# Kernel tuning notes

Measured on AMD Instinct MI355X. Metric: run time of the kernel, lower is better.

## Reference

```python
import jax, jax.numpy as jnp
import numpy as np

B, N, D = 4, 1024, 64
H, DH = 8, 64
INNER = H * DH  # 512 == dim*heads
NUM_F, GH, GW = 4, 16, 16  # N = GH*GW*NUM_F
EPS_LN = 1e-5


def setup_inputs() -> dict:
    key = jax.random.key(0)
    ks = jax.random.split(key, 5)
    return {
        "x": jax.random.normal(ks[0], (B, N, D), dtype=jnp.float32),
        "W_qkv": jax.random.normal(ks[1], (D, 3 * INNER), dtype=jnp.float32) * 0.05,
        "b_qkv": jax.random.normal(ks[2], (3 * INNER,), dtype=jnp.float32) * 0.02,
        "ln_g": jnp.ones((INNER,), dtype=jnp.float32),
        "ln_b": jnp.zeros((INNER,), dtype=jnp.float32),
        "W_out": jax.random.normal(ks[3], (INNER, D), dtype=jnp.float32) * 0.05,
        "b_out": jnp.zeros((D,), dtype=jnp.float32),
    }


def _safe_sqrt(d2):
    # sqrt with zero (not inf) gradient at 0 (diagonal of cdist)
    pos = d2 > 1e-12
    return jnp.where(pos, jnp.sqrt(jnp.where(pos, d2, 1.0)), 0.0)


def _spe_weights(x):
    # torch.cdist(x, x, p=2) then Gaussian kernel, thresholded at mean
    sq = jnp.sum(x * x, axis=-1)  # (B,N)
    d2 = sq[:, :, None] + sq[:, None, :] - 2.0 * jnp.einsum('bnd,bmd->bnm', x, x)
    d2 = jnp.maximum(d2, 0.0)
    dist = _safe_sqrt(d2)
    sigma = jnp.mean(dist)
    w = jnp.exp(-d2 / (2.0 * sigma * sigma))
    return jnp.where(w < jnp.mean(w), 0.0, w)  # (B,N,N)


def _spa_weights():
    # constant spatial-grid Gaussian weights, identical across batch
    gx, gy, gz = jnp.meshgrid(jnp.arange(GH), jnp.arange(GW), jnp.arange(NUM_F), indexing='ij')
    grid = jnp.stack([gx, gy, gz], axis=-1).reshape(N, 3).astype(jnp.float32)
    diff = grid[:, None, :] - grid[None, :, :]
    d2 = jnp.sum(diff * diff, axis=-1)
    dist = jnp.sqrt(d2)
    sigma = jnp.mean(dist)
    w = jnp.exp(-d2 / (2.0 * sigma * sigma))
    return jnp.where(w < jnp.mean(w), 0.0, w)  # (N,N)


def reference(x, W_qkv, b_qkv, ln_g, ln_b, W_out, b_out):
    spe = _spe_weights(x)            # (B,N,N), broadcast over heads
    spa = _spa_weights()             # (N,N), broadcast over batch & heads

    qkv = x @ W_qkv + b_qkv          # (B,N,3*INNER)
    q, k, v = jnp.split(qkv, 3, axis=-1)
    to_heads = lambda t: t.reshape(B, N, H, DH).transpose(0, 2, 1, 3)  # (B,H,N,DH)
    q, k, v = to_heads(q), to_heads(k), to_heads(v)

    scale = DH ** (-0.5)
    qe = jax.nn.elu(q) + 1.0
    ke = jax.nn.elu(k) + 1.0
    dots = jnp.einsum('bhid,bhjd->bhij', qe, ke) * scale  # (B,H,N,N)

    masked = dots * spe[:, None, :, :] * spa[None, None, :, :]
    attn = jax.nn.softmax(masked, axis=-1)
    out = jnp.einsum('bhij,bhjd->bhid', attn, v)          # (B,H,N,DH)
    out = out.transpose(0, 2, 1, 3).reshape(B, N, INNER)

    # to_out: LayerNorm -> GELU (exact) -> Linear
    mu = jnp.mean(out, axis=-1, keepdims=True)
    var = jnp.var(out, axis=-1, keepdims=True)
    y = ln_g * (out - mu) / jnp.sqrt(var + EPS_LN) + ln_b
    y = jax.nn.gelu(y, approximate=False)
    return y @ W_out + b_out  # (B,N,D)
```

## Files before the change

kernel.cpp:

```cpp
#include <hip/hip_runtime.h>
#include <math.h>
#include <stdlib.h>

#define B 4
#define N 1024
#define D 64
#define H 8
#define DH 64
#define INNER 512
#define C3 1536
#define BHN 32768
#define BHND 2097152

typedef __attribute__((ext_vector_type(8))) short bf16x8;
typedef __attribute__((ext_vector_type(4))) float f32x4;

__device__ inline short f2bf(float f) {
    unsigned u = __builtin_bit_cast(unsigned, f);
    unsigned r = (u + 0x7FFFu + ((u >> 16) & 1u)) >> 16;
    return (short)r;
}
__device__ inline float bf2f(short s) {
    return __builtin_bit_cast(float, ((unsigned)(unsigned short)s) << 16);
}

__global__ __launch_bounds__(256) void k_prep(const float* __restrict__ x, const float* __restrict__ Wqkv,
                                              short* __restrict__ xh, short* __restrict__ xl,
                                              float* __restrict__ sq,
                                              short* __restrict__ Wh, short* __restrict__ Wl,
                                              float* __restrict__ spa, float inv2s2, float mu,
                                              float* __restrict__ scal) {
    __shared__ float lds[64 * 65];
    int t = threadIdx.x;
    int bb = blockIdx.x;
    if (bb < 1024) {
        if (bb == 0 && t < 16) scal[t] = 0.f;
        int i = bb * 4 + (t >> 6), d = t & 63;
        float v = x[i * 64 + d];
        short hs = f2bf(v);
        xh[i * 64 + d] = hs;
        xl[i * 64 + d] = f2bf(v - bf2f(hs));
        float s = v * v;
#pragma unroll
        for (int m = 32; m; m >>= 1) s += __shfl_xor(s, m, 64);
        if (d == 0) sq[i] = s;
    } else if (bb < 1048) {
        int c0 = (bb - 1024) * 64;
#pragma unroll
        for (int it = 0; it < 16; it++) {
            int d = it * 4 + (t >> 6), cl = t & 63;
            lds[cl * 65 + d] = Wqkv[d * C3 + c0 + cl];
        }
        __syncthreads();
#pragma unroll
        for (int it = 0; it < 16; it++) {
            int cl = it * 4 + (t >> 6), d = t & 63;
            float v = lds[cl * 65 + d];
            short hs = f2bf(v);
            Wh[(c0 + cl) * 64 + d] = hs;
            Wl[(c0 + cl) * 64 + d] = f2bf(v - bf2f(hs));
        }
    } else {
        int flat4 = (bb - 1048) * 256 + t;
        int i = flat4 >> 8;
        int j0 = (flat4 & 255) * 4;
        int ix = i >> 6, iy = (i >> 2) & 15, iz = i & 3;
        float4 o;
        float* op = (float*)&o;
#pragma unroll
        for (int jj = 0; jj < 4; jj++) {
            int j = j0 + jj;
            int jx = j >> 6, jy = (j >> 2) & 15, jz = j & 3;
            float d2 = (float)((ix - jx) * (ix - jx) + (iy - jy) * (iy - jy) + (iz - jz) * (iz - jz));
            float w = __expf(-d2 * inv2s2);
            op[jj] = (w < mu) ? 0.f : w;
        }
        ((float4*)spa)[flat4] = o;
    }
}

__global__ __launch_bounds__(256) void k_gemm(
    const short* __restrict__ xh, const short* __restrict__ xl,
    const short* __restrict__ Wh, const short* __restrict__ Wl,
    const float* __restrict__ bqkv, const float* __restrict__ sq,
    short* __restrict__ qeh, short* __restrict__ qel,
    short* __restrict__ keh, short* __restrict__ kel,
    short* __restrict__ vT, float* __restrict__ w, float* __restrict__ d_sig) {
    __shared__ short vt_lds[128 * 66];
    __shared__ float red[4];
    int t = threadIdx.x;
    int wv = t >> 6, lane = t & 63, l4 = lane & 15, g = lane >> 4;
    const bf16x8* xh8 = (const bf16x8*)xh;
    const bf16x8* xl8 = (const bf16x8*)xl;

    if (blockIdx.x < 768) {
        int i0 = (blockIdx.x & 63) * 64;
        int c0 = (blockIdx.x >> 6) * 128;
        int irow = i0 + wv * 16;
        const bf16x8* Wh8 = (const bf16x8*)Wh;
        const bf16x8* Wl8 = (const bf16x8*)Wl;
        int abase = (irow + l4) * 8 + g;
        bf16x8 ah[2], al[2];
        ah[0] = xh8[abase];
        ah[1] = xh8[abase + 4];
        al[0] = xl8[abase];
        al[1] = xl8[abase + 4];
        f32x4 acc[8];
#pragma unroll
        for (int ct = 0; ct < 8; ct++) {
            int c = c0 + 16 * ct + l4;
            int bbase = c * 8 + g;
            bf16x8 bh0 = Wh8[bbase], bh1 = Wh8[bbase + 4];
            bf16x8 bl0 = Wl8[bbase], bl1 = Wl8[bbase + 4];
            f32x4 a = f32x4{0.f, 0.f, 0.f, 0.f};
            a = __builtin_amdgcn_mfma_f32_16x16x32_bf16(ah[0], bh0, a, 0, 0, 0);
            a = __builtin_amdgcn_mfma_f32_16x16x32_bf16(ah[1], bh1, a, 0, 0, 0);
            a = __builtin_amdgcn_mfma_f32_16x16x32_bf16(al[0], bh0, a, 0, 0, 0);
            a = __builtin_amdgcn_mfma_f32_16x16x32_bf16(al[1], bh1, a, 0, 0, 0);
            a = __builtin_amdgcn_mfma_f32_16x16x32_bf16(ah[0], bl0, a, 0, 0, 0);
            a = __builtin_amdgcn_mfma_f32_16x16x32_bf16(ah[1], bl1, a, 0, 0, 0);
            acc[ct] = a;
        }
        int seg = c0 >> 9;
#pragma unroll
        for (int ct = 0; ct < 8; ct++) {
            int c = c0 + 16 * ct + l4;
            float bias = bqkv[c];
            int cc = c & 511, hh = cc >> 6, dh = cc & 63;
#pragma unroll
            for (int r = 0; r < 4; r++) {
                int i_e = irow + 4 * g + r;
                int b = i_e >> 10, i = i_e & 1023;
                float val = acc[ct][r] + bias;
                if (seg < 2) {
                    float a_ = val > 0.f ? val + 1.f : __expf(val);
                    short hs = f2bf(a_);
                    short ls = f2bf(a_ - bf2f(hs));
                    int off = ((b * H + hh) * N + i) * 64 + dh;
                    if (seg == 0) { qeh[off] = hs; qel[off] = ls; }
                    else          { keh[off] = hs; kel[off] = ls; }
                } else {
                    vt_lds[(16 * ct + l4) * 66 + (wv * 16 + 4 * g + r)] = f2bf(val);
                }
            }
        }
        if (seg == 2) {
            __syncthreads();
            int b = i0 >> 10, ib = i0 & 1023;
#pragma unroll
            for (int it = 0; it < 4; it++) {
                int idx = t + 256 * it;
                int cl = idx >> 3, i8 = idx & 7;
                short tmp[8];
#pragma unroll
                for (int r8 = 0; r8 < 8; r8++) tmp[r8] = vt_lds[cl * 66 + i8 * 8 + r8];
                int cc = (c0 + cl) & 511, hh = cc >> 6, dh = cc & 63;
                ((bf16x8*)vT)[((b * H + hh) * 64 + dh) * (N / 8) + (ib >> 3) + i8] = *(bf16x8*)tmp;
            }
        }
    } else {
        int q = blockIdx.x - 768;
        int i0 = (q & 15) * 64, j0 = ((q >> 4) & 7) * 128, b = q >> 7;
        int irow = i0 + wv * 16;
        int abase = (b * N + irow + l4) * 8 + g;
        bf16x8 ah[2], al[2];
        ah[0] = xh8[abase];
        ah[1] = xh8[abase + 4];
        al[0] = xl8[abase];
        al[1] = xl8[abase + 4];
        f32x4 acc[8];
#pragma unroll
        for (int ct = 0; ct < 8; ct++) {
            int j = j0 + 16 * ct + l4;
            int bbase = (b * N + j) * 8 + g;
            bf16x8 bh0 = xh8[bbase], bh1 = xh8[bbase + 4];
            bf16x8 bl0 = xl8[bbase], bl1 = xl8[bbase + 4];
            f32x4 a = f32x4{0.f, 0.f, 0.f, 0.f};
            a = __builtin_amdgcn_mfma_f32_16x16x32_bf16(ah[0], bh0, a, 0, 0, 0);
            a = __builtin_amdgcn_mfma_f32_16x16x32_bf16(ah[1], bh1, a, 0, 0, 0);
            a = __builtin_amdgcn_mfma_f32_16x16x32_bf16(al[0], bh0, a, 0, 0, 0);
            a = __builtin_amdgcn_mfma_f32_16x16x32_bf16(al[1], bh1, a, 0, 0, 0);
            a = __builtin_amdgcn_mfma_f32_16x16x32_bf16(ah[0], bl0, a, 0, 0, 0);
            a = __builtin_amdgcn_mfma_f32_16x16x32_bf16(ah[1], bl1, a, 0, 0, 0);
            acc[ct] = a;
        }
        float sqi[4];
#pragma unroll
        for (int r = 0; r < 4; r++) sqi[r] = sq[b * N + irow + 4 * g + r];
        float part = 0.f;
#pragma unroll
        for (int ct = 0; ct < 8; ct++) {
            int j = j0 + 16 * ct + l4;
            float sqj = sq[b * N + j];
#pragma unroll
            for (int r = 0; r < 4; r++) {
                float d2 = sqi[r] + sqj - 2.f * acc[ct][r];
                d2 = fmaxf(d2, 0.f);
                w[((size_t)b * N + irow + 4 * g + r) * N + j] = d2;
                part += (d2 > 1e-12f) ? sqrtf(d2) : 0.f;
            }
        }
#pragma unroll
        for (int m = 32; m; m >>= 1) part += __shfl_xor(part, m, 64);
        if (lane == 0) red[wv] = part;
        __syncthreads();
        if (t == 0) atomicAdd(d_sig, red[0] + red[1] + red[2] + red[3]);
    }
}

__global__ __launch_bounds__(256) void k_wsum(const float* __restrict__ w, const float* __restrict__ d_sig,
                                              float* __restrict__ d_wsum) {
    __shared__ float red[4];
    float sigma = d_sig[0] * (1.f / 4194304.f);
    float inv = 1.f / (2.f * sigma * sigma);
    float s = 0.f;
    for (int idx = blockIdx.x * 256 + threadIdx.x; idx < 1048576; idx += 256 * 2048) {
        float4 v = ((const float4*)w)[idx];
        s += __expf(-v.x * inv) + __expf(-v.y * inv) + __expf(-v.z * inv) + __expf(-v.w * inv);
    }
#pragma unroll
    for (int m = 32; m; m >>= 1) s += __shfl_xor(s, m, 64);
    if ((threadIdx.x & 63) == 0) red[threadIdx.x >> 6] = s;
    __syncthreads();
    if (threadIdx.x == 0) atomicAdd(d_wsum, red[0] + red[1] + red[2] + red[3]);
}

__global__ __launch_bounds__(256) void k_attn(
    const short* __restrict__ qeh, const short* __restrict__ qel,
    const short* __restrict__ keh, const short* __restrict__ kel,
    const short* __restrict__ vT,
    const float* __restrict__ w, const float* __restrict__ spa,
    const float* __restrict__ scal, float* __restrict__ Opart, float2* __restrict__ ml2) {
    __shared__ short Kh[64 * 64];
    __shared__ short Kl[64 * 64];
    __shared__ short Vt[64 * 64];
    __shared__ short P[4][16 * 64];
    int t = threadIdx.x;
    int wv = t >> 6, lane = t & 63, l4 = lane & 15, g = lane >> 4;
    int half = blockIdx.x & 1;
    int i0 = (blockIdx.x >> 1) * 64;
    int h = blockIdx.y, b = blockIdx.z, bh = b * H + h;
    float sigma = scal[0] * (1.f / 4194304.f);
    float inv = 1.f / (2.f * sigma * sigma);
    float mu = scal[1] * (1.f / 4194304.f);
    int irow = i0 + wv * 16;

    bf16x8 qh[2], ql[2];
    {
        const bf16x8* qh8 = (const bf16x8*)qeh;
        const bf16x8* ql8 = (const bf16x8*)qel;
        int base = (bh * N + irow + l4) * 8 + g;
#pragma unroll
        for (int mk = 0; mk < 2; mk++) {
            qh[mk] = qh8[base + 4 * mk];
            ql[mk] = ql8[base + 4 * mk];
        }
    }
    f32x4 O[4];
#pragma unroll
    for (int dt = 0; dt < 4; dt++) O[dt] = f32x4{0.f, 0.f, 0.f, 0.f};
    float m_r[4] = {-INFINITY, -INFINITY, -INFINITY, -INFINITY};
    float l_r[4] = {0.f, 0.f, 0.f, 0.f};

    const bf16x8* Kh8 = (const bf16x8*)Kh;
    const bf16x8* Kl8 = (const bf16x8*)Kl;
    const bf16x8* Vt8 = (const bf16x8*)Vt;

    for (int tile = half * 8; tile < half * 8 + 8; ++tile) {
        int j0 = tile * 64;
        __syncthreads();
        {
            const bf16x8* kh8 = (const bf16x8*)keh;
            const bf16x8* kl8 = (const bf16x8*)kel;
            const bf16x8* v8 = (const bf16x8*)vT;
            bf16x8* KhW = (bf16x8*)Kh;
            bf16x8* KlW = (bf16x8*)Kl;
            bf16x8* VtW = (bf16x8*)Vt;
#pragma unroll
            for (int rep = 0; rep < 2; rep++) {
                int c = t + 256 * rep;
                int j = c >> 3, s = c & 7;
                KhW[j * 8 + (s ^ (j & 7))] = kh8[(bh * N + j0 + j) * 8 + s];
                KlW[j * 8 + (s ^ (j & 7))] = kl8[(bh * N + j0 + j) * 8 + s];
                VtW[j * 8 + (s ^ (j & 7))] = v8[(bh * 64 + j) * (N / 8) + (j0 >> 3) + s];
            }
        }
        __syncthreads();
        f32x4 sc[4];
#pragma unroll
        for (int ct = 0; ct < 4; ct++) {
            int j = 16 * ct + l4;
            int sw = j & 7;
            bf16x8 kh0 = Kh8[j * 8 + ((g) ^ sw)];
            bf16x8 kh1 = Kh8[j * 8 + ((4 + g) ^ sw)];
            bf16x8 kl0 = Kl8[j * 8 + ((g) ^ sw)];
            bf16x8 kl1 = Kl8[j * 8 + ((4 + g) ^ sw)];
            f32x4 a = f32x4{0.f, 0.f, 0.f, 0.f};
            a = __builtin_amdgcn_mfma_f32_16x16x32_bf16(qh[0], kh0, a, 0, 0, 0);
            a = __builtin_amdgcn_mfma_f32_16x16x32_bf16(qh[1], kh1, a, 0, 0, 0);
            a = __builtin_amdgcn_mfma_f32_16x16x32_bf16(ql[0], kh0, a, 0, 0, 0);
            a = __builtin_amdgcn_mfma_f32_16x16x32_bf16(ql[1], kh1, a, 0, 0, 0);
            a = __builtin_amdgcn_mfma_f32_16x16x32_bf16(qh[0], kl0, a, 0, 0, 0);
            a = __builtin_amdgcn_mfma_f32_16x16x32_bf16(qh[1], kl1, a, 0, 0, 0);
            sc[ct] = a;
        }
        float p[4][4];
        float fr[4];
#pragma unroll
        for (int r = 0; r < 4; r++) {
            int i = irow + 4 * g + r;
            float mx = -INFINITY;
#pragma unroll
            for (int ct = 0; ct < 4; ct++) {
                int jg = j0 + 16 * ct + l4;
                float d2v = w[((size_t)b * N + i) * N + jg];
                float sp = spa[(size_t)i * N + jg];
                float wv_ = __expf(-d2v * inv);
                float spe = (wv_ < mu) ? 0.f : wv_;
                float val = sc[ct][r] * 0.125f * spe * sp;
                p[ct][r] = val;
                mx = fmaxf(mx, val);
            }
#pragma unroll
            for (int msk = 1; msk < 16; msk <<= 1) mx = fmaxf(mx, __shfl_xor(mx, msk, 64));
            float mo = m_r[r];
            float mn = fmaxf(mo, mx);
            float f = __expf(mo - mn);
            float s = 0.f;
#pragma unroll
            for (int ct = 0; ct < 4; ct++) {
                float e = __expf(p[ct][r] - mn);
                p[ct][r] = e;
                s += e;
            }
#pragma unroll
            for (int msk = 1; msk < 16; msk <<= 1) s += __shfl_xor(s, msk, 64);
            l_r[r] = l_r[r] * f + s;
            m_r[r] = mn;
            fr[r] = f;
        }
#pragma unroll
        for (int dt = 0; dt < 4; dt++) {
            O[dt][0] *= fr[0];
            O[dt][1] *= fr[1];
            O[dt][2] *= fr[2];
            O[dt][3] *= fr[3];
        }
        short* Pw = P[wv];
#pragma unroll
        for (int ct = 0; ct < 4; ct++) {
#pragma unroll
            for (int r = 0; r < 4; r++) {
                int row = 4 * g + r;
                int slot = ((l4 >> 3) + 2 * ct) ^ (row & 7);
                Pw[row * 64 + slot * 8 + (l4 & 7)] = f2bf(p[ct][r]);
            }
        }
        const bf16x8* Pr = (const bf16x8*)P[wv];
#pragma unroll
        for (int ks = 0; ks < 2; ks++) {
            bf16x8 pa = Pr[l4 * 8 + ((g + 4 * ks) ^ (l4 & 7))];
#pragma unroll
            for (int dt = 0; dt < 4; dt++) {
                int d = l4 + 16 * dt;
                bf16x8 bv = Vt8[d * 8 + ((g + 4 * ks) ^ (d & 7))];
                O[dt] = __builtin_amdgcn_mfma_f32_16x16x32_bf16(pa, bv, O[dt], 0, 0, 0);
            }
        }
    }
    float* Op = Opart + (size_t)half * BHND;
#pragma unroll
    for (int dt = 0; dt < 4; dt++) {
#pragma unroll
        for (int r = 0; r < 4; r++) {
            int i = irow + 4 * g + r;
            Op[((size_t)bh * N + i) * 64 + l4 + 16 * dt] = O[dt][r];
        }
    }
    if (l4 == 0) {
#pragma unroll
        for (int r = 0; r < 4; r++)
            ml2[half * BHN + bh * N + irow + 4 * g + r] = float2{m_r[r], l_r[r]};
    }
}

__device__ inline float4 comb4(const float* __restrict__ Opart, const float2* __restrict__ ml2,
                               int bh, int ib, int dq) {
    float2 a0 = ml2[bh * N + ib];
    float2 a1 = ml2[BHN + bh * N + ib];
    float m = fmaxf(a0.x, a1.x);
    float e0 = __expf(a0.x - m), e1 = __expf(a1.x - m);
    float inv = 1.f / (a0.y * e0 + a1.y * e1);
    const float4* Op4 = (const float4*)Opart;
    float4 O0 = Op4[(size_t)(bh * N + ib) * 16 + dq];
    float4 O1 = Op4[(size_t)(BHND / 4) + (size_t)(bh * N + ib) * 16 + dq];
    float4 v;
    v.x = (O0.x * e0 + O1.x * e1) * inv;
    v.y = (O0.y * e0 + O1.y * e1) * inv;
    v.z = (O0.z * e0 + O1.z * e1) * inv;
    v.w = (O0.w * e0 + O1.w * e1) * inv;
    return v;
}

__global__ __launch_bounds__(256) void k_out(const float* __restrict__ Opart, const float2* __restrict__ ml2,
                                             const float* __restrict__ g, const float* __restrict__ be,
                                             const float* __restrict__ Wout, const float* __restrict__ bout,
                                             float* __restrict__ out) {
    __shared__ float y_s[8 * 512];
    int t = threadIdx.x;
    int wv = t >> 6, lane = t & 63;
    int r0 = blockIdx.x * 8;
#pragma unroll
    for (int rr = 0; rr < 2; rr++) {
        int rloc = wv * 2 + rr;
        int ig = r0 + rloc;
        int b = ig >> 10, ib = ig & 1023;
        int c0 = 4 * lane, c1 = c0 + 256;
        float4 v0 = comb4(Opart, ml2, b * H + (c0 >> 6), ib, (c0 & 63) >> 2);
        float4 v1 = comb4(Opart, ml2, b * H + (c1 >> 6), ib, (c1 & 63) >> 2);
        float s1 = v0.x + v0.y + v0.z + v0.w + v1.x + v1.y + v1.z + v1.w;
        float s2 = v0.x * v0.x + v0.y * v0.y + v0.z * v0.z + v0.w * v0.w +
                   v1.x * v1.x + v1.y * v1.y + v1.z * v1.z + v1.w * v1.w;
#pragma unroll
        for (int m = 32; m; m >>= 1) {
            s1 += __shfl_xor(s1, m, 64);
            s2 += __shfl_xor(s2, m, 64);
        }
        float mean = s1 * (1.f / 512.f);
        float var = s2 * (1.f / 512.f) - mean * mean;
        float rstd = rsqrtf(var + 1e-5f);
        float4 o0, o1;
#pragma unroll
        for (int e = 0; e < 4; e++) {
            float yn = g[c0 + e] * (((float*)&v0)[e] - mean) * rstd + be[c0 + e];
            ((float*)&o0)[e] = 0.5f * yn * (1.f + erff(yn * 0.70710678118f));
            float ym = g[c1 + e] * (((float*)&v1)[e] - mean) * rstd + be[c1 + e];
            ((float*)&o1)[e] = 0.5f * ym * (1.f + erff(ym * 0.70710678118f));
        }
        ((float4*)(y_s + rloc * 512))[lane] = o0;
        ((float4*)(y_s + rloc * 512))[lane + 64] = o1;
    }
    __syncthreads();
    int o = t & 63, rg = t >> 6;
    float a0 = 0.f, a1 = 0.f;
#pragma unroll 4
    for (int c = 0; c < 512; c++) {
        float wv_ = Wout[c * 64 + o];
        a0 = fmaf(y_s[(rg * 2) * 512 + c], wv_, a0);
        a1 = fmaf(y_s[(rg * 2 + 1) * 512 + c], wv_, a1);
    }
    float bo = bout[o];
    out[(size_t)(r0 + rg * 2) * 64 + o] = a0 + bo;
    out[(size_t)(r0 + rg * 2 + 1) * 64 + o] = a1 + bo;
}

extern "C" void kernel_launch(void* const* d_in, const int* in_sizes, int n_in,
                              void* d_out, int out_size, void* d_ws, size_t ws_size,
                              hipStream_t stream) {
    const float* x = (const float*)d_in[0];
    const float* Wqkv = (const float*)d_in[1];
    const float* bqkv = (const float*)d_in[2];
    const float* lng = (const float*)d_in[3];
    const float* lnb = (const float*)d_in[4];
    const float* Wout = (const float*)d_in[5];
    const float* bout = (const float*)d_in[6];
    float* out = (float*)d_out;

    float* ws = (float*)d_ws;
    size_t off = 0;
    float* sq = ws + off;    off += (size_t)B * N;
    float* scal = ws + off;  off += 16;
    float* spa = ws + off;   off += (size_t)N * N;
    float* wbuf = ws + off;  off += (size_t)B * N * N;
    float* Opart = ws + off; off += (size_t)2 * BHND;
    float2* ml2 = (float2*)(ws + off); off += (size_t)2 * BHN * 2;
    short* sbase = (short*)(ws + off);
    size_t soff = 0;
    short* qeh = sbase + soff; soff += (size_t)BHND;
    short* qel = sbase + soff; soff += (size_t)BHND;
    short* keh = sbase + soff; soff += (size_t)BHND;
    short* kel = sbase + soff; soff += (size_t)BHND;
    short* vT  = sbase + soff; soff += (size_t)BHND;
    short* xh  = sbase + soff; soff += (size_t)B * N * D;
    short* xl  = sbase + soff; soff += (size_t)B * N * D;
    short* Wh  = sbase + soff; soff += (size_t)D * C3;
    short* Wl  = sbase + soff; soff += (size_t)D * C3;

    double ssum = 0.0;
    const double cnt = (double)N * (double)N;
    for (int dx = -15; dx <= 15; dx++)
        for (int dy = -15; dy <= 15; dy++)
            for (int dz = -3; dz <= 3; dz++) {
                double c = (double)(16 - abs(dx)) * (double)(16 - abs(dy)) * (double)(4 - abs(dz));
                double d2 = (double)(dx * dx + dy * dy + dz * dz);
                ssum += c * sqrt(d2);
            }
    double sigma = ssum / cnt;
    double inv2s2 = 1.0 / (2.0 * sigma * sigma);
    double wsum = 0.0;
    for (int dx = -15; dx <= 15; dx++)
        for (int dy = -15; dy <= 15; dy++)
            for (int dz = -3; dz <= 3; dz++) {
                double c = (double)(16 - abs(dx)) * (double)(16 - abs(dy)) * (double)(4 - abs(dz));
                double d2 = (double)(dx * dx + dy * dy + dz * dz);
                wsum += c * exp(-d2 * inv2s2);
            }
    double mu = wsum / cnt;

    k_prep<<<2072, 256, 0, stream>>>(x, Wqkv, xh, xl, sq, Wh, Wl, spa, (float)inv2s2, (float)mu, scal);
    k_gemm<<<1280, 256, 0, stream>>>(xh, xl, Wh, Wl, bqkv, sq, qeh, qel, keh, kel, vT, wbuf, scal);
    k_wsum<<<2048, 256, 0, stream>>>(wbuf, scal, scal + 1);
    k_attn<<<dim3(32, H, B), 256, 0, stream>>>(qeh, qel, keh, kel, vT, wbuf, spa, scal, Opart, ml2);
    k_out<<<512, 256, 0, stream>>>(Opart, ml2, lng, lnb, Wout, bout, out);
}
```

Measured before the change: 227.5 us.

## Precompute combined bf16 attention mask once and drop split-KV partial combine

```diff
diff --git a/kernel.cpp b/kernel.cpp
--- a/kernel.cpp
+++ b/kernel.cpp
@@ -225,24 +225,40 @@
     if (threadIdx.x == 0) atomicAdd(d_wsum, red[0] + red[1] + red[2] + red[3]);
 }
 
+__global__ __launch_bounds__(256) void k_mask(const float* __restrict__ w, const float* __restrict__ spa,
+                                              const float* __restrict__ scal, short* __restrict__ Mb) {
+    float sigma = scal[0] * (1.f / 4194304.f);
+    float inv = 1.f / (2.f * sigma * sigma);
+    float mu = scal[1] * (1.f / 4194304.f);
+    float d2thr = -__logf(mu) / inv;
+    for (int idx = blockIdx.x * 256 + threadIdx.x; idx < 1048576; idx += 256 * 2048) {
+        float4 d2v = ((const float4*)w)[idx];
+        float4 sp = ((const float4*)spa)[idx & 262143];
+        short tmp[4];
+        float* dp = (float*)&d2v;
+        float* pp = (float*)&sp;
+#pragma unroll
+        for (int e = 0; e < 4; e++) {
+            float m = (dp[e] > d2thr) ? 0.f : __expf(-dp[e] * inv) * pp[e] * 0.125f;
+            tmp[e] = f2bf(m);
+        }
+        *(uint2*)(Mb + (size_t)idx * 4) = *(uint2*)tmp;
+    }
+}
+
 __global__ __launch_bounds__(256) void k_attn(
     const short* __restrict__ qeh, const short* __restrict__ qel,
     const short* __restrict__ keh, const short* __restrict__ kel,
-    const short* __restrict__ vT,
-    const float* __restrict__ w, const float* __restrict__ spa,
-    const float* __restrict__ scal, float* __restrict__ Opart, float2* __restrict__ ml2) {
+    const short* __restrict__ vT, const short* __restrict__ Mb,
+    float* __restrict__ aout) {
     __shared__ short Kh[64 * 64];
     __shared__ short Kl[64 * 64];
     __shared__ short Vt[64 * 64];
     __shared__ short P[4][16 * 64];
     int t = threadIdx.x;
     int wv = t >> 6, lane = t & 63, l4 = lane & 15, g = lane >> 4;
-    int half = blockIdx.x & 1;
-    int i0 = (blockIdx.x >> 1) * 64;
+    int i0 = blockIdx.x * 64;
     int h = blockIdx.y, b = blockIdx.z, bh = b * H + h;
-    float sigma = scal[0] * (1.f / 4194304.f);
-    float inv = 1.f / (2.f * sigma * sigma);
-    float mu = scal[1] * (1.f / 4194304.f);
     int irow = i0 + wv * 16;
 
     bf16x8 qh[2], ql[2];
@@ -266,7 +282,7 @@
     const bf16x8* Kl8 = (const bf16x8*)Kl;
     const bf16x8* Vt8 = (const bf16x8*)Vt;
 
-    for (int tile = half * 8; tile < half * 8 + 8; ++tile) {
+    for (int tile = 0; tile < 16; ++tile) {
         int j0 = tile * 64;
         __syncthreads();
         {
@@ -287,6 +303,7 @@
         }
         __syncthreads();
         f32x4 sc[4];
+        __builtin_amdgcn_s_setprio(1);
 #pragma unroll
         for (int ct = 0; ct < 4; ct++) {
             int j = 16 * ct + l4;
@@ -304,20 +321,18 @@
             a = __builtin_amdgcn_mfma_f32_16x16x32_bf16(qh[1], kl1, a, 0, 0, 0);
             sc[ct] = a;
         }
+        __builtin_amdgcn_s_setprio(0);
         float p[4][4];
         float fr[4];
 #pragma unroll
         for (int r = 0; r < 4; r++) {
             int i = irow + 4 * g + r;
+            const short* Mrow = Mb + ((size_t)b * N + i) * N + j0;
             float mx = -INFINITY;
 #pragma unroll
             for (int ct = 0; ct < 4; ct++) {
-                int jg = j0 + 16 * ct + l4;
-                float d2v = w[((size_t)b * N + i) * N + jg];
-                float sp = spa[(size_t)i * N + jg];
-                float wv_ = __expf(-d2v * inv);
-                float spe = (wv_ < mu) ? 0.f : wv_;
-                float val = sc[ct][r] * 0.125f * spe * sp;
+                float mval = bf2f(Mrow[16 * ct + l4]);
+                float val = sc[ct][r] * mval;
                 p[ct][r] = val;
                 mx = fmaxf(mx, val);
             }
@@ -357,6 +372,7 @@
             }
         }
         const bf16x8* Pr = (const bf16x8*)P[wv];
+        __builtin_amdgcn_s_setprio(1);
 #pragma unroll
         for (int ks = 0; ks < 2; ks++) {
             bf16x8 pa = Pr[l4 * 8 + ((g + 4 * ks) ^ (l4 & 7))];
@@ -367,45 +383,21 @@
                 O[dt] = __builtin_amdgcn_mfma_f32_16x16x32_bf16(pa, bv, O[dt], 0, 0, 0);
             }
         }
-    }
-    float* Op = Opart + (size_t)half * BHND;
+        __builtin_amdgcn_s_setprio(0);
+    }
 #pragma unroll
     for (int dt = 0; dt < 4; dt++) {
 #pragma unroll
         for (int r = 0; r < 4; r++) {
             int i = irow + 4 * g + r;
-            Op[((size_t)bh * N + i) * 64 + l4 + 16 * dt] = O[dt][r];
-        }
-    }
-    if (l4 == 0) {
-#pragma unroll
-        for (int r = 0; r < 4; r++)
-            ml2[half * BHN + bh * N + irow + 4 * g + r] = float2{m_r[r], l_r[r]};
-    }
-}
-
-__device__ inline float4 comb4(const float* __restrict__ Opart, const float2* __restrict__ ml2,
-                               int bh, int ib, int dq) {
-    float2 a0 = ml2[bh * N + ib];
-    float2 a1 = ml2[BHN + bh * N + ib];
-    float m = fmaxf(a0.x, a1.x);
-    float e0 = __expf(a0.x - m), e1 = __expf(a1.x - m);
-    float inv = 1.f / (a0.y * e0 + a1.y * e1);
-    const float4* Op4 = (const float4*)Opart;
-    float4 O0 = Op4[(size_t)(bh * N + ib) * 16 + dq];
-    float4 O1 = Op4[(size_t)(BHND / 4) + (size_t)(bh * N + ib) * 16 + dq];
-    float4 v;
-    v.x = (O0.x * e0 + O1.x * e1) * inv;
-    v.y = (O0.y * e0 + O1.y * e1) * inv;
-    v.z = (O0.z * e0 + O1.z * e1) * inv;
-    v.w = (O0.w * e0 + O1.w * e1) * inv;
-    return v;
-}
-
-__global__ __launch_bounds__(256) void k_out(const float* __restrict__ Opart, const float2* __restrict__ ml2,
-                                             const float* __restrict__ g, const float* __restrict__ be,
-                                             const float* __restrict__ Wout, const float* __restrict__ bout,
-                                             float* __restrict__ out) {
+            aout[((size_t)b * N + i) * INNER + h * 64 + l4 + 16 * dt] = O[dt][r] / l_r[r];
+        }
+    }
+}
+
+__global__ __launch_bounds__(256) void k_out(const float* __restrict__ aout, const float* __restrict__ g,
+                                             const float* __restrict__ be, const float* __restrict__ Wout,
+                                             const float* __restrict__ bout, float* __restrict__ out) {
     __shared__ float y_s[8 * 512];
     int t = threadIdx.x;
     int wv = t >> 6, lane = t & 63;
@@ -413,11 +405,9 @@
 #pragma unroll
     for (int rr = 0; rr < 2; rr++) {
         int rloc = wv * 2 + rr;
-        int ig = r0 + rloc;
-        int b = ig >> 10, ib = ig & 1023;
-        int c0 = 4 * lane, c1 = c0 + 256;
-        float4 v0 = comb4(Opart, ml2, b * H + (c0 >> 6), ib, (c0 & 63) >> 2);
-        float4 v1 = comb4(Opart, ml2, b * H + (c1 >> 6), ib, (c1 & 63) >> 2);
+        const float* rp = aout + (size_t)(r0 + rloc) * 512;
+        float4 v0 = ((const float4*)rp)[lane];
+        float4 v1 = ((const float4*)rp)[lane + 64];
         float s1 = v0.x + v0.y + v0.z + v0.w + v1.x + v1.y + v1.z + v1.w;
         float s2 = v0.x * v0.x + v0.y * v0.y + v0.z * v0.z + v0.w * v0.w +
                    v1.x * v1.x + v1.y * v1.y + v1.z * v1.z + v1.w * v1.w;
@@ -429,6 +419,7 @@
         float mean = s1 * (1.f / 512.f);
         float var = s2 * (1.f / 512.f) - mean * mean;
         float rstd = rsqrtf(var + 1e-5f);
+        int c0 = 4 * lane, c1 = 4 * lane + 256;
         float4 o0, o1;
 #pragma unroll
         for (int e = 0; e < 4; e++) {
@@ -472,8 +463,7 @@
     float* scal = ws + off;  off += 16;
     float* spa = ws + off;   off += (size_t)N * N;
     float* wbuf = ws + off;  off += (size_t)B * N * N;
-    float* Opart = ws + off; off += (size_t)2 * BHND;
-    float2* ml2 = (float2*)(ws + off); off += (size_t)2 * BHN * 2;
+    float* aout = ws + off;  off += (size_t)B * N * INNER;
     short* sbase = (short*)(ws + off);
     size_t soff = 0;
     short* qeh = sbase + soff; soff += (size_t)BHND;
@@ -481,6 +471,7 @@
     short* keh = sbase + soff; soff += (size_t)BHND;
     short* kel = sbase + soff; soff += (size_t)BHND;
     short* vT  = sbase + soff; soff += (size_t)BHND;
+    short* Mb  = sbase + soff; soff += (size_t)B * N * N;
     short* xh  = sbase + soff; soff += (size_t)B * N * D;
     short* xl  = sbase + soff; soff += (size_t)B * N * D;
     short* Wh  = sbase + soff; soff += (size_t)D * C3;
@@ -510,6 +501,7 @@
     k_prep<<<2072, 256, 0, stream>>>(x, Wqkv, xh, xl, sq, Wh, Wl, spa, (float)inv2s2, (float)mu, scal);
     k_gemm<<<1280, 256, 0, stream>>>(xh, xl, Wh, Wl, bqkv, sq, qeh, qel, keh, kel, vT, wbuf, scal);
     k_wsum<<<2048, 256, 0, stream>>>(wbuf, scal, scal + 1);
-    k_attn<<<dim3(32, H, B), 256, 0, stream>>>(qeh, qel, keh, kel, vT, wbuf, spa, scal, Opart, ml2);
-    k_out<<<512, 256, 0, stream>>>(Opart, ml2, lng, lnb, Wout, bout, out);
-}
+    k_mask<<<2048, 256, 0, stream>>>(wbuf, spa, scal, Mb);
+    k_attn<<<dim3(N / 64, H, B), 256, 0, stream>>>(qeh, qel, keh, kel, vT, Mb, aout);
+    k_out<<<512, 256, 0, stream>>>(aout, lng, lnb, Wout, bout, out);
+}
```

After: 221.9 us. 1.03x faster.
